# Performance work log

Hardware: AMD Instinct MI355X
Metric: run time of the kernel (lower is better)

## Reference

```python
import jax, jax.numpy as jnp
import numpy as np

EPS = 1e-06

def feature_map(x):
    # elu(x) + 1, strictly positive
    return jax.nn.elu(x) + 1.0

def setup_inputs() -> dict:
    key = jax.random.key(0)
    k1, k2, k3 = jax.random.split(key, 3)
    n, s, h, d = 8, 8192, 8, 64
    return {
        "queries": jax.random.normal(k1, (n, s, h, d), dtype=jnp.float32),
        "keys": jax.random.normal(k2, (n, s, h, d), dtype=jnp.float32),
        "values": jax.random.normal(k3, (n, s, h, d), dtype=jnp.float32),
        "h": 128,
        "w": 64,
    }

def reference(queries, keys, values, h, w):
    Q = feature_map(queries)            # [n, l, h, d]
    K = feature_map(keys)               # [n, s, h, d]
    # KV outer-product summed over sequence: [n, h, m, d]
    KV = jnp.einsum('nshd,nshm->nhmd', K, values)
    # normalizer: Q . sum_s K   -> [n, l, h]
    Z = 1.0 / (jnp.einsum('nlhd,nhd->nlh', Q, K.sum(axis=1)) + EPS)
    # output: [n, l, h, m]
    V = jnp.einsum('nlhd,nhmd,nlh->nlhm', Q, KV, Z)
    return V
```

## Files before the change

kernel.cpp:

```cpp
#include <hip/hip_runtime.h>
#include <math.h>


#define N_B 8
#define S_LEN 8192
#define H_N 8
#define D_DIM 64
#define NH (N_B * H_N)
#define EPS 1e-6f
#define ROWSTRIDE (H_N * D_DIM)
#define NCHUNK 16
#define TS 32
#define TILES (S_LEN / NCHUNK / TS)

typedef __attribute__((ext_vector_type(8)))  __bf16 bf16x8;
typedef __attribute__((ext_vector_type(4)))  float  f32x4;
typedef __attribute__((ext_vector_type(4)))  int    i32x4;

__device__ __forceinline__ float felu1(float x) {
    return x > 0.0f ? x + 1.0f : __expf(x);
}

__global__ __launch_bounds__(256) void kv_partial_kernel(
        const float* __restrict__ Kin, const float* __restrict__ Vin,
        float* __restrict__ kvp,
        float* __restrict__ ksp) {
    __shared__ __align__(16) unsigned int KT[2][64 * 32];
    __shared__ __align__(16) unsigned int VT[2][64 * 32];

    const int b    = blockIdx.x;
    const int h_i  = b & 7;
    const int rest = b >> 3;
    const int c    = rest & (NCHUNK - 1);
    const int n_i  = rest >> 4;
    const int nh   = n_i * H_N + h_i;
    const int ob   = nh * NCHUNK + c;
    const int s0   = c * (S_LEN / NCHUNK);

    const int t = threadIdx.x;
    const int w = t >> 6;
    const int l = t & 63;
    const int d = l;

    const float* Kb = Kin + (size_t)n_i * S_LEN * ROWSTRIDE + (size_t)h_i * D_DIM;
    const float* Vb = Vin + (size_t)n_i * S_LEN * ROWSTRIDE + (size_t)h_i * D_DIM;

    float kraw[8], vraw[8];
    float ksum = 0.0f;

    auto issue = [&](int tile) {
        const int sr = s0 + tile * TS + w * 8;
        #pragma unroll
        for (int e = 0; e < 8; ++e) {
            kraw[e] = Kb[(size_t)(sr + e) * ROWSTRIDE + d];
            vraw[e] = Vb[(size_t)(sr + e) * ROWSTRIDE + d];
        }
    };

    auto convert_write = [&](int buf) {
        unsigned int kh[4], kl[4], vh[4], vl[4];
        #pragma unroll
        for (int p = 0; p < 4; ++p) {
            const float x0 = felu1(kraw[2 * p]);
            const float x1 = felu1(kraw[2 * p + 1]);
            ksum += x0 + x1;
            const unsigned u0 = __float_as_uint(x0), u1 = __float_as_uint(x1);
            const unsigned h0 = u0 & 0xFFFF0000u,    h1 = u1 & 0xFFFF0000u;
            const float r0 = x0 - __uint_as_float(h0);
            const float r1 = x1 - __uint_as_float(h1);
            kh[p] = (h0 >> 16) | h1;
            kl[p] = (__float_as_uint(r0) >> 16) | (__float_as_uint(r1) & 0xFFFF0000u);
            const float y0 = vraw[2 * p], y1 = vraw[2 * p + 1];
            const unsigned q0 = __float_as_uint(y0), q1 = __float_as_uint(y1);
            const unsigned g0 = q0 & 0xFFFF0000u,    g1 = q1 & 0xFFFF0000u;
            const float z0 = y0 - __uint_as_float(g0);
            const float z1 = y1 - __uint_as_float(g1);
            vh[p] = (g0 >> 16) | g1;
            vl[p] = (__float_as_uint(z0) >> 16) | (__float_as_uint(z1) & 0xFFFF0000u);
        }
        const int ph = ((w)     ^ (d & 7)) * 4;
        const int pl = ((w + 4) ^ (d & 7)) * 4;
        unsigned int* kr = &KT[buf][d * 32];
        unsigned int* vr = &VT[buf][d * 32];
        *(i32x4*)&kr[ph] = (i32x4){(int)kh[0], (int)kh[1], (int)kh[2], (int)kh[3]};
        *(i32x4*)&kr[pl] = (i32x4){(int)kl[0], (int)kl[1], (int)kl[2], (int)kl[3]};
        *(i32x4*)&vr[ph] = (i32x4){(int)vh[0], (int)vh[1], (int)vh[2], (int)vh[3]};
        *(i32x4*)&vr[pl] = (i32x4){(int)vl[0], (int)vl[1], (int)vl[2], (int)vl[3]};
    };

    f32x4 acc0 = {0.f, 0.f, 0.f, 0.f};
    f32x4 acc1 = {0.f, 0.f, 0.f, 0.f};
    f32x4 acc2 = {0.f, 0.f, 0.f, 0.f};
    f32x4 acc3 = {0.f, 0.f, 0.f, 0.f};

    const int arow = 16 * w + (l & 15);
    const int ghi  = ((l >> 4) ^ (l & 7));
    const int glo  = ((4 + (l >> 4)) ^ (l & 7));
    const int aoff_h = arow * 32 + ghi * 4;
    const int aoff_l = arow * 32 + glo * 4;
    const int brow0  = (l & 15) * 32;

    issue(0);
    convert_write(0);
    __syncthreads();

    int cur = 0;
    for (int tile = 0; tile < TILES; ++tile) {
        const bool more = (tile + 1 < TILES);
        if (more) issue(tile + 1);

        const bf16x8 Ahi = __builtin_bit_cast(bf16x8, *(const i32x4*)&KT[cur][aoff_h]);
        const bf16x8 Alo = __builtin_bit_cast(bf16x8, *(const i32x4*)&KT[cur][aoff_l]);
        #pragma unroll
        for (int mt = 0; mt < 4; ++mt) {
            const int bo = brow0 + mt * 16 * 32;
            const bf16x8 Bhi = __builtin_bit_cast(bf16x8, *(const i32x4*)&VT[cur][bo + ghi * 4]);
            const bf16x8 Blo = __builtin_bit_cast(bf16x8, *(const i32x4*)&VT[cur][bo + glo * 4]);
            f32x4* acc = (mt == 0) ? &acc0 : (mt == 1) ? &acc1 : (mt == 2) ? &acc2 : &acc3;
            *acc = __builtin_amdgcn_mfma_f32_16x16x32_bf16(Ahi, Bhi, *acc, 0, 0, 0);
            *acc = __builtin_amdgcn_mfma_f32_16x16x32_bf16(Ahi, Blo, *acc, 0, 0, 0);
            *acc = __builtin_amdgcn_mfma_f32_16x16x32_bf16(Alo, Bhi, *acc, 0, 0, 0);
        }

        if (more) convert_write(cur ^ 1);
        __syncthreads();
        cur ^= 1;
    }

    float* kvo = kvp + (size_t)ob * (D_DIM * D_DIM);
    #pragma unroll
    for (int mt = 0; mt < 4; ++mt) {
        const f32x4 a = (mt == 0) ? acc0 : (mt == 1) ? acc1 : (mt == 2) ? acc2 : acc3;
        #pragma unroll
        for (int r = 0; r < 4; ++r) {
            const int row = 16 * w + (l >> 4) * 4 + r;
            const int col = 16 * mt + (l & 15);
            kvo[row * 64 + col] = a[r];
        }
    }

    float* ksl = (float*)&KT[0][0];
    __syncthreads();
    ksl[w * 64 + d] = ksum;
    __syncthreads();
    if (t < D_DIM) {
        ksp[(size_t)ob * D_DIM + t] =
            ksl[t] + ksl[64 + t] + ksl[128 + t] + ksl[192 + t];
    }
}

__global__ __launch_bounds__(256) void kv_reduce_kernel(
        const float* __restrict__ kvp, const float* __restrict__ ksp,
        float* __restrict__ KV, float* __restrict__ Ksum) {
    const int nh = blockIdx.x >> 4;
    const int eb = blockIdx.x & 15;
    const int t  = threadIdx.x;
    const int e  = eb * 256 + t;
    float s = 0.0f;
    const float* base = kvp + (size_t)nh * NCHUNK * (D_DIM * D_DIM) + e;
    #pragma unroll
    for (int c = 0; c < NCHUNK; ++c)
        s += base[(size_t)c * (D_DIM * D_DIM)];
    KV[(size_t)nh * (D_DIM * D_DIM) + e] = s;
    if (eb == 0 && t < D_DIM) {
        float ks = 0.0f;
        const float* kb = ksp + (size_t)nh * NCHUNK * D_DIM + t;
        #pragma unroll
        for (int c = 0; c < NCHUNK; ++c) ks += kb[(size_t)c * D_DIM];
        Ksum[(size_t)nh * D_DIM + t] = ks;
    }
}

__global__ __launch_bounds__(256) void out_kernel(
        const float* __restrict__ Qin, const float* __restrict__ KV,
        const float* __restrict__ Ksum, float* __restrict__ Out) {
    constexpr int RPB  = 128;
    constexpr int QPAD = 68;
    __shared__ __align__(16) float KVs[D_DIM][D_DIM];
    __shared__ __align__(16) float Kss[D_DIM];
    __shared__ __align__(16) float Qs[RPB][QPAD];

    const int b    = blockIdx.x;
    const int nblk = S_LEN / RPB;
    const int h_i  = b & 7;
    const int rest = b >> 3;
    const int rb   = rest & (nblk - 1);
    const int n_i  = rest >> 6;
    const int nh   = n_i * H_N + h_i;
    const int t    = threadIdx.x;

    const float* Qb = Qin + (size_t)n_i * S_LEN * ROWSTRIDE + (size_t)h_i * D_DIM;
    float*       Ob = Out + (size_t)n_i * S_LEN * ROWSTRIDE + (size_t)h_i * D_DIM;

    {
        const float4* src = (const float4*)(KV + (size_t)nh * (D_DIM * D_DIM));
        float4* dst = (float4*)(&KVs[0][0]);
        #pragma unroll
        for (int i = 0; i < 4; ++i) dst[t + 256 * i] = src[t + 256 * i];
        if (t < 16) ((float4*)Kss)[t] = ((const float4*)(Ksum + (size_t)nh * D_DIM))[t];
    }

    const int ltx = t & 15, lty = t >> 4;
    const int sbase = rb * RPB;
    #pragma unroll
    for (int i = 0; i < 8; ++i) {
        const int row = lty + 16 * i;
        const float4 q = *(const float4*)(Qb + (size_t)(sbase + row) * ROWSTRIDE + ltx * 4);
        float4 f;
        f.x = felu1(q.x); f.y = felu1(q.y); f.z = felu1(q.z); f.w = felu1(q.w);
        const int pc = (ltx * 4) ^ (((row >> 2) & 7) << 2);
        *(float4*)&Qs[row][pc] = f;
    }
    __syncthreads();

    const int rg = t >> 3;
    const int mg = t & 7;
    const int r0 = rg * 4, m0 = mg * 8;
    const int sw = ((rg & 7) << 2);

    float acc[4][8];
    float zz[4];
    #pragma unroll
    for (int r = 0; r < 4; ++r) {
        zz[r] = 0.0f;
        #pragma unroll
        for (int m = 0; m < 8; ++m) acc[r][m] = 0.0f;
    }

    #pragma unroll
    for (int d0 = 0; d0 < D_DIM; d0 += 4) {
        const float4 ks4 = *(const float4*)&Kss[d0];
        float4 qr[4];
        #pragma unroll
        for (int r = 0; r < 4; ++r) {
            qr[r] = *(const float4*)&Qs[r0 + r][d0 ^ sw];
            zz[r] += qr[r].x * ks4.x + qr[r].y * ks4.y
                   + qr[r].z * ks4.z + qr[r].w * ks4.w;
        }
        #pragma unroll
        for (int j = 0; j < 4; ++j) {
            const float4 kva = *(const float4*)&KVs[d0 + j][m0];
            const float4 kvb = *(const float4*)&KVs[d0 + j][m0 + 4];
            #pragma unroll
            for (int r = 0; r < 4; ++r) {
                const float q = (&qr[r].x)[j];
                acc[r][0] += q * kva.x; acc[r][1] += q * kva.y;
                acc[r][2] += q * kva.z; acc[r][3] += q * kva.w;
                acc[r][4] += q * kvb.x; acc[r][5] += q * kvb.y;
                acc[r][6] += q * kvb.z; acc[r][7] += q * kvb.w;
            }
        }
    }

    #pragma unroll
    for (int r = 0; r < 4; ++r) {
        const float z = 1.0f / (zz[r] + EPS);
        float4 o1, o2;
        o1.x = acc[r][0] * z; o1.y = acc[r][1] * z;
        o1.z = acc[r][2] * z; o1.w = acc[r][3] * z;
        o2.x = acc[r][4] * z; o2.y = acc[r][5] * z;
        o2.z = acc[r][6] * z; o2.w = acc[r][7] * z;
        float* op = Ob + (size_t)(sbase + r0 + r) * ROWSTRIDE + m0;
        *(float4*)op       = o1;
        *(float4*)(op + 4) = o2;
    }
}

extern "C" void kernel_launch(void* const* d_in, const int* in_sizes, int n_in,
                              void* d_out, int out_size, void* d_ws, size_t ws_size,
                              hipStream_t stream) {
    const float* q = (const float*)d_in[0];
    const float* k = (const float*)d_in[1];
    const float* v = (const float*)d_in[2];
    float* out = (float*)d_out;

    float* kvp  = (float*)d_ws;
    float* ksp  = kvp + (size_t)NH * NCHUNK * D_DIM * D_DIM;
    float* KVf  = ksp + (size_t)NH * NCHUNK * D_DIM;
    float* Ksum = KVf + (size_t)NH * D_DIM * D_DIM;

    kv_partial_kernel<<<NH * NCHUNK, 256, 0, stream>>>(k, v, kvp, ksp);
    kv_reduce_kernel<<<NH * 16, 256, 0, stream>>>(kvp, ksp, KVf, Ksum);
    out_kernel<<<NH * (S_LEN / 128), 256, 0, stream>>>(q, KVf, Ksum, out);
}
```

Before: 155.4 us.

## Drop split-bf16 compensation, double chunk count, and deepen KV load pipeline

```diff
diff --git a/kernel.cpp b/kernel.cpp
--- a/kernel.cpp
+++ b/kernel.cpp
@@ -9,9 +9,10 @@
 #define NH (N_B * H_N)
 #define EPS 1e-6f
 #define ROWSTRIDE (H_N * D_DIM)
-#define NCHUNK 16
-#define TS 32
-#define TILES (S_LEN / NCHUNK / TS)
+#define NCHUNK 32
+#define CROWS (S_LEN / NCHUNK)
+#define TS 64
+#define TILES (CROWS / TS)
 
 typedef __attribute__((ext_vector_type(8)))  __bf16 bf16x8;
 typedef __attribute__((ext_vector_type(4)))  float  f32x4;
@@ -19,6 +20,13 @@
 
 __device__ __forceinline__ float felu1(float x) {
     return x > 0.0f ? x + 1.0f : __expf(x);
+}
+__device__ __forceinline__ unsigned bfb(float f) {
+    __bf16 h = (__bf16)f;
+    return (unsigned)__builtin_bit_cast(unsigned short, h);
+}
+__device__ __forceinline__ int pack2bf(float a, float b) {
+    return (int)(bfb(a) | (bfb(b) << 16));
 }
 
 __global__ __launch_bounds__(256) void kv_partial_kernel(
@@ -32,10 +40,10 @@
     const int h_i  = b & 7;
     const int rest = b >> 3;
     const int c    = rest & (NCHUNK - 1);
-    const int n_i  = rest >> 4;
+    const int n_i  = rest >> 5;
     const int nh   = n_i * H_N + h_i;
     const int ob   = nh * NCHUNK + c;
-    const int s0   = c * (S_LEN / NCHUNK);
+    const int s0   = c * CROWS;
 
     const int t = threadIdx.x;
     const int w = t >> 6;
@@ -45,102 +53,94 @@
     const float* Kb = Kin + (size_t)n_i * S_LEN * ROWSTRIDE + (size_t)h_i * D_DIM;
     const float* Vb = Vin + (size_t)n_i * S_LEN * ROWSTRIDE + (size_t)h_i * D_DIM;
 
-    float kraw[8], vraw[8];
+    float kraw[16], vraw[16];
     float ksum = 0.0f;
 
     auto issue = [&](int tile) {
-        const int sr = s0 + tile * TS + w * 8;
+        const size_t base = (size_t)(s0 + tile * TS + w * 8) * ROWSTRIDE + d;
         #pragma unroll
         for (int e = 0; e < 8; ++e) {
-            kraw[e] = Kb[(size_t)(sr + e) * ROWSTRIDE + d];
-            vraw[e] = Vb[(size_t)(sr + e) * ROWSTRIDE + d];
+            kraw[e] = Kb[base + (size_t)e * ROWSTRIDE];
+            vraw[e] = Vb[base + (size_t)e * ROWSTRIDE];
+        }
+        #pragma unroll
+        for (int e = 0; e < 8; ++e) {
+            kraw[8 + e] = Kb[base + (size_t)(32 + e) * ROWSTRIDE];
+            vraw[8 + e] = Vb[base + (size_t)(32 + e) * ROWSTRIDE];
         }
     };
 
-    auto convert_write = [&](int buf) {
-        unsigned int kh[4], kl[4], vh[4], vl[4];
+    auto convwrite = [&](int buf) {
+        int kp[8], vp[8];
         #pragma unroll
         for (int p = 0; p < 4; ++p) {
-            const float x0 = felu1(kraw[2 * p]);
-            const float x1 = felu1(kraw[2 * p + 1]);
-            ksum += x0 + x1;
-            const unsigned u0 = __float_as_uint(x0), u1 = __float_as_uint(x1);
-            const unsigned h0 = u0 & 0xFFFF0000u,    h1 = u1 & 0xFFFF0000u;
-            const float r0 = x0 - __uint_as_float(h0);
-            const float r1 = x1 - __uint_as_float(h1);
-            kh[p] = (h0 >> 16) | h1;
-            kl[p] = (__float_as_uint(r0) >> 16) | (__float_as_uint(r1) & 0xFFFF0000u);
-            const float y0 = vraw[2 * p], y1 = vraw[2 * p + 1];
-            const unsigned q0 = __float_as_uint(y0), q1 = __float_as_uint(y1);
-            const unsigned g0 = q0 & 0xFFFF0000u,    g1 = q1 & 0xFFFF0000u;
-            const float z0 = y0 - __uint_as_float(g0);
-            const float z1 = y1 - __uint_as_float(g1);
-            vh[p] = (g0 >> 16) | g1;
-            vl[p] = (__float_as_uint(z0) >> 16) | (__float_as_uint(z1) & 0xFFFF0000u);
-        }
-        const int ph = ((w)     ^ (d & 7)) * 4;
-        const int pl = ((w + 4) ^ (d & 7)) * 4;
+            const float a0 = felu1(kraw[2 * p]);
+            const float a1 = felu1(kraw[2 * p + 1]);
+            const float b0 = felu1(kraw[8 + 2 * p]);
+            const float b1 = felu1(kraw[8 + 2 * p + 1]);
+            ksum += (a0 + a1) + (b0 + b1);
+            kp[p]     = pack2bf(a0, a1);
+            kp[4 + p] = pack2bf(b0, b1);
+            vp[p]     = pack2bf(vraw[2 * p],     vraw[2 * p + 1]);
+            vp[4 + p] = pack2bf(vraw[8 + 2 * p], vraw[8 + 2 * p + 1]);
+        }
+        const int gA = ((w)     ^ (d & 7)) * 4;
+        const int gB = ((w + 4) ^ (d & 7)) * 4;
         unsigned int* kr = &KT[buf][d * 32];
         unsigned int* vr = &VT[buf][d * 32];
-        *(i32x4*)&kr[ph] = (i32x4){(int)kh[0], (int)kh[1], (int)kh[2], (int)kh[3]};
-        *(i32x4*)&kr[pl] = (i32x4){(int)kl[0], (int)kl[1], (int)kl[2], (int)kl[3]};
-        *(i32x4*)&vr[ph] = (i32x4){(int)vh[0], (int)vh[1], (int)vh[2], (int)vh[3]};
-        *(i32x4*)&vr[pl] = (i32x4){(int)vl[0], (int)vl[1], (int)vl[2], (int)vl[3]};
+        *(i32x4*)&kr[gA] = (i32x4){kp[0], kp[1], kp[2], kp[3]};
+        *(i32x4*)&kr[gB] = (i32x4){kp[4], kp[5], kp[6], kp[7]};
+        *(i32x4*)&vr[gA] = (i32x4){vp[0], vp[1], vp[2], vp[3]};
+        *(i32x4*)&vr[gB] = (i32x4){vp[4], vp[5], vp[6], vp[7]};
     };
 
-    f32x4 acc0 = {0.f, 0.f, 0.f, 0.f};
-    f32x4 acc1 = {0.f, 0.f, 0.f, 0.f};
-    f32x4 acc2 = {0.f, 0.f, 0.f, 0.f};
-    f32x4 acc3 = {0.f, 0.f, 0.f, 0.f};
+    f32x4 acc[4];
+    #pragma unroll
+    for (int i = 0; i < 4; ++i) acc[i] = (f32x4){0.f, 0.f, 0.f, 0.f};
 
     const int arow = 16 * w + (l & 15);
-    const int ghi  = ((l >> 4) ^ (l & 7));
-    const int glo  = ((4 + (l >> 4)) ^ (l & 7));
-    const int aoff_h = arow * 32 + ghi * 4;
-    const int aoff_l = arow * 32 + glo * 4;
-    const int brow0  = (l & 15) * 32;
+    const int g0   = (((l >> 4))     ^ (l & 7)) * 4;
+    const int g1   = ((4 + (l >> 4)) ^ (l & 7)) * 4;
+    const int brow = (l & 15);
+
+    auto compute = [&](int buf) {
+        const bf16x8 A0 = __builtin_bit_cast(bf16x8, *(const i32x4*)&KT[buf][arow * 32 + g0]);
+        const bf16x8 A1 = __builtin_bit_cast(bf16x8, *(const i32x4*)&KT[buf][arow * 32 + g1]);
+        #pragma unroll
+        for (int mt = 0; mt < 4; ++mt) {
+            const int br = (16 * mt + brow) * 32;
+            const bf16x8 B0 = __builtin_bit_cast(bf16x8, *(const i32x4*)&VT[buf][br + g0]);
+            const bf16x8 B1 = __builtin_bit_cast(bf16x8, *(const i32x4*)&VT[buf][br + g1]);
+            acc[mt] = __builtin_amdgcn_mfma_f32_16x16x32_bf16(A0, B0, acc[mt], 0, 0, 0);
+            acc[mt] = __builtin_amdgcn_mfma_f32_16x16x32_bf16(A1, B1, acc[mt], 0, 0, 0);
+        }
+    };
 
     issue(0);
-    convert_write(0);
+    convwrite(0);
+    issue(1);
     __syncthreads();
 
-    int cur = 0;
     for (int tile = 0; tile < TILES; ++tile) {
-        const bool more = (tile + 1 < TILES);
-        if (more) issue(tile + 1);
-
-        const bf16x8 Ahi = __builtin_bit_cast(bf16x8, *(const i32x4*)&KT[cur][aoff_h]);
-        const bf16x8 Alo = __builtin_bit_cast(bf16x8, *(const i32x4*)&KT[cur][aoff_l]);
-        #pragma unroll
-        for (int mt = 0; mt < 4; ++mt) {
-            const int bo = brow0 + mt * 16 * 32;
-            const bf16x8 Bhi = __builtin_bit_cast(bf16x8, *(const i32x4*)&VT[cur][bo + ghi * 4]);
-            const bf16x8 Blo = __builtin_bit_cast(bf16x8, *(const i32x4*)&VT[cur][bo + glo * 4]);
-            f32x4* acc = (mt == 0) ? &acc0 : (mt == 1) ? &acc1 : (mt == 2) ? &acc2 : &acc3;
-            *acc = __builtin_amdgcn_mfma_f32_16x16x32_bf16(Ahi, Bhi, *acc, 0, 0, 0);
-            *acc = __builtin_amdgcn_mfma_f32_16x16x32_bf16(Ahi, Blo, *acc, 0, 0, 0);
-            *acc = __builtin_amdgcn_mfma_f32_16x16x32_bf16(Alo, Bhi, *acc, 0, 0, 0);
-        }
-
-        if (more) convert_write(cur ^ 1);
+        const int cur = tile & 1;
+        compute(cur);
+        if (tile + 1 < TILES) convwrite(cur ^ 1);
+        if (tile + 2 < TILES) issue(tile + 2);
         __syncthreads();
-        cur ^= 1;
     }
 
     float* kvo = kvp + (size_t)ob * (D_DIM * D_DIM);
     #pragma unroll
     for (int mt = 0; mt < 4; ++mt) {
-        const f32x4 a = (mt == 0) ? acc0 : (mt == 1) ? acc1 : (mt == 2) ? acc2 : acc3;
         #pragma unroll
         for (int r = 0; r < 4; ++r) {
             const int row = 16 * w + (l >> 4) * 4 + r;
             const int col = 16 * mt + (l & 15);
-            kvo[row * 64 + col] = a[r];
+            kvo[row * 64 + col] = acc[mt][r];
         }
     }
 
     float* ksl = (float*)&KT[0][0];
-    __syncthreads();
     ksl[w * 64 + d] = ksum;
     __syncthreads();
     if (t < D_DIM) {
@@ -158,15 +158,15 @@
     const int e  = eb * 256 + t;
     float s = 0.0f;
     const float* base = kvp + (size_t)nh * NCHUNK * (D_DIM * D_DIM) + e;
-    #pragma unroll
+    #pragma unroll 8
     for (int c = 0; c < NCHUNK; ++c)
         s += base[(size_t)c * (D_DIM * D_DIM)];
     KV[(size_t)nh * (D_DIM * D_DIM) + e] = s;
     if (eb == 0 && t < D_DIM) {
         float ks = 0.0f;
-        const float* kb = ksp + (size_t)nh * NCHUNK * D_DIM + t;
-        #pragma unroll
-        for (int c = 0; c < NCHUNK; ++c) ks += kb[(size_t)c * D_DIM];
+        #pragma unroll 8
+        for (int c = 0; c < NCHUNK; ++c)
+            ks += ksp[(size_t)nh * NCHUNK * D_DIM + (size_t)c * D_DIM + t];
         Ksum[(size_t)nh * D_DIM + t] = ks;
     }
 }
@@ -279,7 +279,7 @@
     float* KVf  = ksp + (size_t)NH * NCHUNK * D_DIM;
     float* Ksum = KVf + (size_t)NH * D_DIM * D_DIM;
 
-    kv_partial_kernel<<<NH * NCHUNK, 256, 0, stream>>>(k, v, kvp, ksp);
+    kv_partial_kernel<<<N_B * NCHUNK * H_N, 256, 0, stream>>>(k, v, kvp, ksp);
     kv_reduce_kernel<<<NH * 16, 256, 0, stream>>>(kvp, ksp, KVf, Ksum);
     out_kernel<<<NH * (S_LEN / 128), 256, 0, stream>>>(q, KVf, Ksum, out);
 }
```

Result: slower. 170.4 us (+9.6%).
